# Optimization experiments

Hardware: AMD Instinct MI355X
Metric: run time of the kernel (lower is better)

## Reference

```python
import jax, jax.numpy as jnp
import numpy as np

F = 6      # num_factors (== nodes per sample)
H = 32     # hidden_dim
B = 65536  # batch of samples (vectorized version of the per-sample Python loop)


def setup_inputs() -> dict:
    key = jax.random.key(0)
    ks = jax.random.split(key, 20)
    p = lambda k, shape: (jax.random.normal(k, shape, dtype=jnp.float32) * 0.1)
    inp = {
        "factors": jax.random.normal(ks[0], (B, F, F), dtype=jnp.float32),
        # CausalStructureLearner.node_encoder: Linear(F, H)
        "Wn": p(ks[1], (F, H)), "bn": p(ks[2], (H,)),
        # edge_predictor: Linear(2H, H) -> ReLU -> Linear(H, 1) -> Sigmoid
        "We1": p(ks[3], (2 * H, H)), "be1": p(ks[4], (H,)),
        "We2": p(ks[5], (H, 1)), "be2": p(ks[6], (1,)),
        # DynamicsPredictor.dynamics_net: F->H->H->F
        "Wd1": p(ks[7], (F, H)), "bd1": p(ks[8], (H,)),
        "Wd2": p(ks[9], (H, H)), "bd2": p(ks[10], (H,)),
        "Wd3": p(ks[11], (H, F)), "bd3": p(ks[12], (F,)),
        # AnomalyScorer.score_net: 3F->32->16->1 -> Sigmoid
        "Ws1": p(ks[13], (3 * F, 32)), "bs1": p(ks[14], (32,)),
        "Ws2": p(ks[15], (32, 16)), "bs2": p(ks[16], (16,)),
        "Ws3": p(ks[17], (16, 1)), "bs3": p(ks[18], (1,)),
    }
    return inp


def reference(factors, Wn, bn, We1, be1, We2, be2,
              Wd1, bd1, Wd2, bd2, Wd3, bd3,
              Ws1, bs1, Ws2, bs2, Ws3, bs3):
    # --- CausalStructureLearner (vectorized pairwise edge scoring) ---
    nf = factors @ Wn + bn                                  # [B, F, H]
    src = jnp.broadcast_to(nf[:, :, None, :], (B, F, F, H))  # node i
    dst = jnp.broadcast_to(nf[:, None, :, :], (B, F, F, H))  # node j
    pair = jnp.concatenate([src, dst], axis=-1)             # [B, F, F, 2H]
    eh = jax.nn.relu(pair @ We1 + be1)                       # [B, F, F, H]
    adj = jax.nn.sigmoid((eh @ We2 + be2)[..., 0])           # [B, F, F]
    adj = adj * (1.0 - jnp.eye(F, dtype=adj.dtype))          # zero diagonal

    # --- DynamicsPredictor: (adj @ factors.T).T == factors @ adj^T ---
    structured = jnp.einsum('bij,bnj->bni', adj, factors)    # [B, F(nodes), F]
    h = jax.nn.relu(structured @ Wd1 + bd1)
    h = jax.nn.relu(h @ Wd2 + bd2)
    pred = h @ Wd3 + bd3                                     # [B, F, F]

    # --- AnomalyScorer ---
    diff = jnp.abs(factors - pred)
    si = jnp.concatenate([factors, pred, diff], axis=-1)     # [B, F, 3F]
    s = jax.nn.relu(si @ Ws1 + bs1)
    s = jax.nn.relu(s @ Ws2 + bs2)
    s = jax.nn.sigmoid(s @ Ws3 + bs3)                        # [B, F, 1]
    scores = jnp.mean(s, axis=(1, 2))                        # [B]

    return adj, pred, scores
```

## Files before the change

### kernel.cpp

```cpp
#include <hip/hip_runtime.h>
#include <math.h>

#define NT  256
#define SPB 84

#define O_REC  0
#define O_WD1  512
#define O_BD1  704
#define O_WD2  736
#define O_BD2  1760
#define O_WD3T 1792
#define O_BD3  1984
#define O_WS1  1992
#define O_BS1  2568
#define O_WS2  2600
#define O_BS2  3112
#define O_WS3  3128
#define O_MISC 3144
#define W_TOT  3148

#define ADJ_STRIDE 52

__device__ __forceinline__ float sigmoidf_(float x) {
    return 1.0f / (1.0f + __expf(-x));
}

__global__ __launch_bounds__(NT, 1) void fused3_kernel(
        const float* __restrict__ factors,
        const float* __restrict__ Wn,  const float* __restrict__ bn,
        const float* __restrict__ We1, const float* __restrict__ be1,
        const float* __restrict__ We2, const float* __restrict__ be2,
        const float* __restrict__ Wd1, const float* __restrict__ bd1,
        const float* __restrict__ Wd2, const float* __restrict__ bd2,
        const float* __restrict__ Wd3, const float* __restrict__ bd3,
        const float* __restrict__ Ws1, const float* __restrict__ bs1,
        const float* __restrict__ Ws2, const float* __restrict__ bs2,
        const float* __restrict__ Ws3, const float* __restrict__ bs3,
        float* __restrict__ adj_out, float* __restrict__ pred_out,
        float* __restrict__ scores, int B) {
    __shared__ float Wsh[W_TOT];
    __shared__ float adj_s[SPB * ADJ_STRIDE];
    __shared__ float sc_s[SPB * 6];

    const int t = threadIdx.x;
    const int s = t / 3;
    const int n = t - s * 3;
    const int b = blockIdx.x * SPB + s;
    const bool act = (t < SPB * 3);
    const int sl_ = (s < SPB) ? s : (SPB - 1);
    const bool bv = act && (b < B);

    float fall[36], fi0[6], fi1[6];
    #pragma unroll
    for (int q = 0; q < 36; ++q) fall[q] = 0.f;
    #pragma unroll
    for (int m = 0; m < 6; ++m) { fi0[m] = 0.f; fi1[m] = 0.f; }
    if (bv) {
        const float* f = factors + (size_t)b * 36;
        #pragma unroll
        for (int q = 0; q < 9; ++q) {
            float4 v = reinterpret_cast<const float4*>(f)[q];
            fall[q*4+0] = v.x; fall[q*4+1] = v.y; fall[q*4+2] = v.z; fall[q*4+3] = v.w;
        }
        const float* fr0 = f + n * 6;
        const float* fr1 = fr0 + 18;
        #pragma unroll
        for (int q = 0; q < 3; ++q) {
            float2 v0 = reinterpret_cast<const float2*>(fr0)[q];
            float2 v1 = reinterpret_cast<const float2*>(fr1)[q];
            fi0[q*2+0] = v0.x; fi0[q*2+1] = v0.y;
            fi1[q*2+0] = v1.x; fi1[q*2+1] = v1.y;
        }
    }

    #pragma unroll
    for (int e0 = 0; e0 < 512; e0 += NT) {
        int e = e0 + t;
        int h = e >> 4, sl = e & 15;
        float val = 0.0f;
        if (sl < 6) {
            #pragma unroll
            for (int k = 0; k < 32; ++k) val = fmaf(Wn[sl*32+k], We1[k*32+h], val);
        } else if (sl < 12) {
            int m = sl - 6;
            #pragma unroll
            for (int k = 0; k < 32; ++k) val = fmaf(Wn[m*32+k], We1[(32+k)*32+h], val);
        } else if (sl == 12) {
            #pragma unroll
            for (int k = 0; k < 32; ++k) val = fmaf(bn[k], We1[k*32+h] + We1[(32+k)*32+h], val);
            val += be1[h];
        } else if (sl == 13) {
            val = We2[h];
        }
        Wsh[O_REC + e] = val;
    }
    for (int i = t; i < 192;  i += NT) Wsh[O_WD1 + i] = Wd1[i];
    for (int i = t; i < 1024; i += NT) Wsh[O_WD2 + i] = Wd2[i];
    for (int i = t; i < 192;  i += NT) { int j = i >> 5, k = i & 31; Wsh[O_WD3T + i] = Wd3[k*6 + j]; }
    for (int i = t; i < 576;  i += NT) Wsh[O_WS1 + i] = Ws1[i];
    for (int i = t; i < 512;  i += NT) Wsh[O_WS2 + i] = Ws2[i];
    if (t < 32) Wsh[O_BD1 + t] = bd1[t];
    if (t < 32) Wsh[O_BD2 + t] = bd2[t];
    if (t < 6)  Wsh[O_BD3 + t] = bd3[t];
    if (t < 32) Wsh[O_BS1 + t] = bs1[t];
    if (t < 16) Wsh[O_BS2 + t] = bs2[t];
    if (t < 16) Wsh[O_WS3 + t] = Ws3[t];
    if (t == 0) { Wsh[O_MISC] = bs3[0]; Wsh[O_MISC + 1] = be2[0]; }
    __syncthreads();

    float av0[6], av1[6];
    {
        float acc0[6] = {0.f,0.f,0.f,0.f,0.f,0.f};
        float acc1[6] = {0.f,0.f,0.f,0.f,0.f,0.f};
        #pragma unroll 2
        for (int h = 0; h < 32; ++h) {
            const float* r = &Wsh[O_REC + (h << 4)];
            const float4 r0 = *reinterpret_cast<const float4*>(&r[0]);
            const float4 r1 = *reinterpret_cast<const float4*>(&r[4]);
            const float4 r2 = *reinterpret_cast<const float4*>(&r[8]);
            const float4 r3 = *reinterpret_cast<const float4*>(&r[12]);
            float uh0 = r3.x, uh1 = r3.x;
            uh0 = fmaf(fi0[0], r0.x, uh0); uh1 = fmaf(fi1[0], r0.x, uh1);
            uh0 = fmaf(fi0[1], r0.y, uh0); uh1 = fmaf(fi1[1], r0.y, uh1);
            uh0 = fmaf(fi0[2], r0.z, uh0); uh1 = fmaf(fi1[2], r0.z, uh1);
            uh0 = fmaf(fi0[3], r0.w, uh0); uh1 = fmaf(fi1[3], r0.w, uh1);
            uh0 = fmaf(fi0[4], r1.x, uh0); uh1 = fmaf(fi1[4], r1.x, uh1);
            uh0 = fmaf(fi0[5], r1.y, uh0); uh1 = fmaf(fi1[5], r1.y, uh1);
            const float w2 = r3.y;
            #pragma unroll
            for (int j = 0; j < 6; ++j) {
                float vj =      fall[j*6+0] * r1.z;
                vj = fmaf(fall[j*6+1], r1.w, vj);
                vj = fmaf(fall[j*6+2], r2.x, vj);
                vj = fmaf(fall[j*6+3], r2.y, vj);
                vj = fmaf(fall[j*6+4], r2.z, vj);
                vj = fmaf(fall[j*6+5], r2.w, vj);
                acc0[j] = fmaf(fmaxf(uh0 + vj, 0.f), w2, acc0[j]);
                acc1[j] = fmaf(fmaxf(uh1 + vj, 0.f), w2, acc1[j]);
            }
        }
        const float b2 = Wsh[O_MISC + 1];
        #pragma unroll
        for (int j = 0; j < 6; ++j) {
            av0[j] = (j == n)     ? 0.f : sigmoidf_(acc0[j] + b2);
            av1[j] = (j == n + 3) ? 0.f : sigmoidf_(acc1[j] + b2);
        }
    }
    if (act) {
        float* as = &adj_s[sl_ * ADJ_STRIDE];
        *reinterpret_cast<float4*>(&as[n*8])       = make_float4(av0[0], av0[1], av0[2], av0[3]);
        *reinterpret_cast<float2*>(&as[n*8+4])     = make_float2(av0[4], av0[5]);
        *reinterpret_cast<float4*>(&as[(n+3)*8])   = make_float4(av1[0], av1[1], av1[2], av1[3]);
        *reinterpret_cast<float2*>(&as[(n+3)*8+4]) = make_float2(av1[4], av1[5]);
    }
    if (bv) {
        float* ao = adj_out + (size_t)b * 36 + n * 6;
        *reinterpret_cast<float2*>(&ao[0])  = make_float2(av0[0], av0[1]);
        *reinterpret_cast<float2*>(&ao[2])  = make_float2(av0[2], av0[3]);
        *reinterpret_cast<float2*>(&ao[4])  = make_float2(av0[4], av0[5]);
        *reinterpret_cast<float2*>(&ao[18]) = make_float2(av1[0], av1[1]);
        *reinterpret_cast<float2*>(&ao[20]) = make_float2(av1[2], av1[3]);
        *reinterpret_cast<float2*>(&ao[22]) = make_float2(av1[4], av1[5]);
    }
    __syncthreads();

    float pra[6], prb[6];
    float h2a[32], h2b[32];
    {
        float st0[6], st1[6];
        {
            const float* as = &adj_s[sl_ * ADJ_STRIDE];
            #pragma unroll
            for (int i = 0; i < 6; ++i) {
                const float4 qa = *reinterpret_cast<const float4*>(&as[i*8]);
                const float2 qb = *reinterpret_cast<const float2*>(&as[i*8+4]);
                float v = fi0[0] * qa.x;
                v = fmaf(fi0[1], qa.y, v); v = fmaf(fi0[2], qa.z, v);
                v = fmaf(fi0[3], qa.w, v); v = fmaf(fi0[4], qb.x, v);
                v = fmaf(fi0[5], qb.y, v);
                st0[i] = v;
                float w = fi1[0] * qa.x;
                w = fmaf(fi1[1], qa.y, w); w = fmaf(fi1[2], qa.z, w);
                w = fmaf(fi1[3], qa.w, w); w = fmaf(fi1[4], qb.x, w);
                w = fmaf(fi1[5], qb.y, w);
                st1[i] = w;
            }
        }

        float h1a[32], h1b[32];
        #pragma unroll
        for (int o4 = 0; o4 < 8; ++o4) {
            const float4 v = *reinterpret_cast<const float4*>(&Wsh[O_BD1 + o4*4]);
            h1a[o4*4+0] = v.x; h1a[o4*4+1] = v.y; h1a[o4*4+2] = v.z; h1a[o4*4+3] = v.w;
            h1b[o4*4+0] = v.x; h1b[o4*4+1] = v.y; h1b[o4*4+2] = v.z; h1b[o4*4+3] = v.w;
        }
        #pragma unroll
        for (int m = 0; m < 6; ++m) {
            const float sa = st0[m], sb = st1[m];
            #pragma unroll
            for (int o4 = 0; o4 < 8; ++o4) {
                const float4 w = *reinterpret_cast<const float4*>(&Wsh[O_WD1 + m*32 + o4*4]);
                h1a[o4*4+0] = fmaf(sa, w.x, h1a[o4*4+0]); h1b[o4*4+0] = fmaf(sb, w.x, h1b[o4*4+0]);
                h1a[o4*4+1] = fmaf(sa, w.y, h1a[o4*4+1]); h1b[o4*4+1] = fmaf(sb, w.y, h1b[o4*4+1]);
                h1a[o4*4+2] = fmaf(sa, w.z, h1a[o4*4+2]); h1b[o4*4+2] = fmaf(sb, w.z, h1b[o4*4+2]);
                h1a[o4*4+3] = fmaf(sa, w.w, h1a[o4*4+3]); h1b[o4*4+3] = fmaf(sb, w.w, h1b[o4*4+3]);
            }
        }
        #pragma unroll
        for (int o = 0; o < 32; ++o) { h1a[o] = fmaxf(h1a[o], 0.f); h1b[o] = fmaxf(h1b[o], 0.f); }

        #pragma unroll
        for (int o4 = 0; o4 < 8; ++o4) {
            const float4 v = *reinterpret_cast<const float4*>(&Wsh[O_BD2 + o4*4]);
            h2a[o4*4+0] = v.x; h2a[o4*4+1] = v.y; h2a[o4*4+2] = v.z; h2a[o4*4+3] = v.w;
            h2b[o4*4+0] = v.x; h2b[o4*4+1] = v.y; h2b[o4*4+2] = v.z; h2b[o4*4+3] = v.w;
        }
        #pragma unroll
        for (int k = 0; k < 32; ++k) {
            const float xa = h1a[k], xb = h1b[k];
            #pragma unroll
            for (int o4 = 0; o4 < 8; ++o4) {
                const float4 w = *reinterpret_cast<const float4*>(&Wsh[O_WD2 + k*32 + o4*4]);
                h2a[o4*4+0] = fmaf(xa, w.x, h2a[o4*4+0]); h2b[o4*4+0] = fmaf(xb, w.x, h2b[o4*4+0]);
                h2a[o4*4+1] = fmaf(xa, w.y, h2a[o4*4+1]); h2b[o4*4+1] = fmaf(xb, w.y, h2b[o4*4+1]);
                h2a[o4*4+2] = fmaf(xa, w.z, h2a[o4*4+2]); h2b[o4*4+2] = fmaf(xb, w.z, h2b[o4*4+2]);
                h2a[o4*4+3] = fmaf(xa, w.w, h2a[o4*4+3]); h2b[o4*4+3] = fmaf(xb, w.w, h2b[o4*4+3]);
            }
        }
        #pragma unroll
        for (int o = 0; o < 32; ++o) { h2a[o] = fmaxf(h2a[o], 0.f); h2b[o] = fmaxf(h2b[o], 0.f); }
    }

    #pragma unroll
    for (int j = 0; j < 6; ++j) {
        float va = Wsh[O_BD3 + j], vb = va;
        #pragma unroll
        for (int k4 = 0; k4 < 8; ++k4) {
            const float4 w = *reinterpret_cast<const float4*>(&Wsh[O_WD3T + j*32 + k4*4]);
            va = fmaf(h2a[k4*4+0], w.x, va); vb = fmaf(h2b[k4*4+0], w.x, vb);
            va = fmaf(h2a[k4*4+1], w.y, va); vb = fmaf(h2b[k4*4+1], w.y, vb);
            va = fmaf(h2a[k4*4+2], w.z, va); vb = fmaf(h2b[k4*4+2], w.z, vb);
            va = fmaf(h2a[k4*4+3], w.w, va); vb = fmaf(h2b[k4*4+3], w.w, vb);
        }
        pra[j] = va; prb[j] = vb;
    }
    if (bv) {
        float* po = pred_out + (size_t)b * 36 + n * 6;
        *reinterpret_cast<float2*>(&po[0])  = make_float2(pra[0], pra[1]);
        *reinterpret_cast<float2*>(&po[2])  = make_float2(pra[2], pra[3]);
        *reinterpret_cast<float2*>(&po[4])  = make_float2(pra[4], pra[5]);
        *reinterpret_cast<float2*>(&po[18]) = make_float2(prb[0], prb[1]);
        *reinterpret_cast<float2*>(&po[20]) = make_float2(prb[2], prb[3]);
        *reinterpret_cast<float2*>(&po[22]) = make_float2(prb[4], prb[5]);
    }

    {
        float dfa[6], dfb[6];
        #pragma unroll
        for (int j = 0; j < 6; ++j) { dfa[j] = fabsf(fi0[j] - pra[j]); dfb[j] = fabsf(fi1[j] - prb[j]); }

        float s1a[32], s1b[32];
        #pragma unroll
        for (int o4 = 0; o4 < 8; ++o4) {
            const float4 v = *reinterpret_cast<const float4*>(&Wsh[O_BS1 + o4*4]);
            s1a[o4*4+0] = v.x; s1a[o4*4+1] = v.y; s1a[o4*4+2] = v.z; s1a[o4*4+3] = v.w;
            s1b[o4*4+0] = v.x; s1b[o4*4+1] = v.y; s1b[o4*4+2] = v.z; s1b[o4*4+3] = v.w;
        }
        #pragma unroll
        for (int m = 0; m < 6; ++m) {
            const float aa = fi0[m], pa = pra[m], da = dfa[m];
            const float ab = fi1[m], pb = prb[m], db = dfb[m];
            #pragma unroll
            for (int o4 = 0; o4 < 8; ++o4) {
                const float4 wa = *reinterpret_cast<const float4*>(&Wsh[O_WS1 + m*32 + o4*4]);
                const float4 wp = *reinterpret_cast<const float4*>(&Wsh[O_WS1 + (6+m)*32 + o4*4]);
                const float4 wd = *reinterpret_cast<const float4*>(&Wsh[O_WS1 + (12+m)*32 + o4*4]);
                s1a[o4*4+0] = fmaf(aa, wa.x, fmaf(pa, wp.x, fmaf(da, wd.x, s1a[o4*4+0])));
                s1b[o4*4+0] = fmaf(ab, wa.x, fmaf(pb, wp.x, fmaf(db, wd.x, s1b[o4*4+0])));
                s1a[o4*4+1] = fmaf(aa, wa.y, fmaf(pa, wp.y, fmaf(da, wd.y, s1a[o4*4+1])));
                s1b[o4*4+1] = fmaf(ab, wa.y, fmaf(pb, wp.y, fmaf(db, wd.y, s1b[o4*4+1])));
                s1a[o4*4+2] = fmaf(aa, wa.z, fmaf(pa, wp.z, fmaf(da, wd.z, s1a[o4*4+2])));
                s1b[o4*4+2] = fmaf(ab, wa.z, fmaf(pb, wp.z, fmaf(db, wd.z, s1b[o4*4+2])));
                s1a[o4*4+3] = fmaf(aa, wa.w, fmaf(pa, wp.w, fmaf(da, wd.w, s1a[o4*4+3])));
                s1b[o4*4+3] = fmaf(ab, wa.w, fmaf(pb, wp.w, fmaf(db, wd.w, s1b[o4*4+3])));
            }
        }
        #pragma unroll
        for (int o = 0; o < 32; ++o) { s1a[o] = fmaxf(s1a[o], 0.f); s1b[o] = fmaxf(s1b[o], 0.f); }

        float s2a[16], s2b[16];
        #pragma unroll
        for (int o4 = 0; o4 < 4; ++o4) {
            const float4 v = *reinterpret_cast<const float4*>(&Wsh[O_BS2 + o4*4]);
            s2a[o4*4+0] = v.x; s2a[o4*4+1] = v.y; s2a[o4*4+2] = v.z; s2a[o4*4+3] = v.w;
            s2b[o4*4+0] = v.x; s2b[o4*4+1] = v.y; s2b[o4*4+2] = v.z; s2b[o4*4+3] = v.w;
        }
        #pragma unroll
        for (int k = 0; k < 32; ++k) {
            const float xa = s1a[k], xb = s1b[k];
            #pragma unroll
            for (int o4 = 0; o4 < 4; ++o4) {
                const float4 w = *reinterpret_cast<const float4*>(&Wsh[O_WS2 + k*16 + o4*4]);
                s2a[o4*4+0] = fmaf(xa, w.x, s2a[o4*4+0]); s2b[o4*4+0] = fmaf(xb, w.x, s2b[o4*4+0]);
                s2a[o4*4+1] = fmaf(xa, w.y, s2a[o4*4+1]); s2b[o4*4+1] = fmaf(xb, w.y, s2b[o4*4+1]);
                s2a[o4*4+2] = fmaf(xa, w.z, s2a[o4*4+2]); s2b[o4*4+2] = fmaf(xb, w.z, s2b[o4*4+2]);
                s2a[o4*4+3] = fmaf(xa, w.w, s2a[o4*4+3]); s2b[o4*4+3] = fmaf(xb, w.w, s2b[o4*4+3]);
            }
        }
        #pragma unroll
        for (int o = 0; o < 16; ++o) { s2a[o] = fmaxf(s2a[o], 0.f); s2b[o] = fmaxf(s2b[o], 0.f); }

        float s3a = Wsh[O_MISC], s3b = s3a;
        #pragma unroll
        for (int k4 = 0; k4 < 4; ++k4) {
            const float4 w = *reinterpret_cast<const float4*>(&Wsh[O_WS3 + k4*4]);
            s3a = fmaf(s2a[k4*4+0], w.x, s3a); s3b = fmaf(s2b[k4*4+0], w.x, s3b);
            s3a = fmaf(s2a[k4*4+1], w.y, s3a); s3b = fmaf(s2b[k4*4+1], w.y, s3b);
            s3a = fmaf(s2a[k4*4+2], w.z, s3a); s3b = fmaf(s2b[k4*4+2], w.z, s3b);
            s3a = fmaf(s2a[k4*4+3], w.w, s3a); s3b = fmaf(s2b[k4*4+3], w.w, s3b);
        }
        if (act) {
            sc_s[sl_*6 + n]     = sigmoidf_(s3a);
            sc_s[sl_*6 + n + 3] = sigmoidf_(s3b);
        }
    }
    __syncthreads();

    if (bv && n == 0) {
        float sum = sc_s[sl_*6+0] + sc_s[sl_*6+1] + sc_s[sl_*6+2]
                  + sc_s[sl_*6+3] + sc_s[sl_*6+4] + sc_s[sl_*6+5];
        scores[b] = sum * (1.0f / 6.0f);
    }
}

extern "C" void kernel_launch(void* const* d_in, const int* in_sizes, int n_in,
                              void* d_out, int out_size, void* d_ws, size_t ws_size,
                              hipStream_t stream) {
    const float* factors = (const float*)d_in[0];
    const float* Wn  = (const float*)d_in[1];
    const float* bn  = (const float*)d_in[2];
    const float* We1 = (const float*)d_in[3];
    const float* be1 = (const float*)d_in[4];
    const float* We2 = (const float*)d_in[5];
    const float* be2 = (const float*)d_in[6];
    const float* Wd1 = (const float*)d_in[7];
    const float* bd1 = (const float*)d_in[8];
    const float* Wd2 = (const float*)d_in[9];
    const float* bd2 = (const float*)d_in[10];
    const float* Wd3 = (const float*)d_in[11];
    const float* bd3 = (const float*)d_in[12];
    const float* Ws1 = (const float*)d_in[13];
    const float* bs1 = (const float*)d_in[14];
    const float* Ws2 = (const float*)d_in[15];
    const float* bs2 = (const float*)d_in[16];
    const float* Ws3 = (const float*)d_in[17];
    const float* bs3 = (const float*)d_in[18];

    int B = in_sizes[0] / 36;

    float* adj_out  = (float*)d_out;
    float* pred_out = (float*)d_out + (size_t)B * 36;
    float* scores   = (float*)d_out + (size_t)B * 72;

    int nblocks = (B + SPB - 1) / SPB;
    hipLaunchKernelGGL(fused3_kernel, dim3(nblocks), dim3(NT), 0, stream,
                       factors, Wn, bn, We1, be1, We2, be2,
                       Wd1, bd1, Wd2, bd2, Wd3, bd3,
                       Ws1, bs1, Ws2, bs2, Ws3, bs3,
                       adj_out, pred_out, scores, B);
}
```

Baseline: 179.7 us.

## Precompute folded weights once in a prologue kernel and store them as fp16

A single-block prologue kernel now folds the node encoder into the edge MLP and packs every weight matrix as fp16 (biases stay fp32) into a workspace buffer. The main kernel loads that buffer with float4 copies instead of having each of ~780 blocks redo the 32-term weight folding and the scattered weight loads. Shared-memory weight reads shrink to half8 vectors that are converted to fp32 for the FMAs. This removes redundant per-block setup and halves LDS traffic for weights, in exchange for an extra kernel launch, conversion instructions in the inner loops and fp16 rounding of the weights.

```diff
diff --git a/kernel.cpp b/kernel.cpp
--- a/kernel.cpp
+++ b/kernel.cpp
@@ -1,23 +1,25 @@
 #include <hip/hip_runtime.h>
 #include <math.h>
 
+typedef _Float16 half8 __attribute__((ext_vector_type(8)));
+
 #define NT  256
 #define SPB 84
 
-#define O_REC  0
-#define O_WD1  512
-#define O_BD1  704
-#define O_WD2  736
-#define O_BD2  1760
-#define O_WD3T 1792
-#define O_BD3  1984
-#define O_WS1  1992
-#define O_BS1  2568
-#define O_WS2  2600
-#define O_BS2  3112
-#define O_WS3  3128
-#define O_MISC 3144
-#define W_TOT  3148
+#define FH_REC   0
+#define FH_WD1   256
+#define FH_WD2   352
+#define FH_WD3T  864
+#define FH_WS1   960
+#define FH_WS2   1248
+#define FH_WS3   1504
+#define FF_BD1   1512
+#define FF_BD2   1544
+#define FF_BD3   1576
+#define FF_BS1   1584
+#define FF_BS2   1616
+#define FF_MISC  1632
+#define W_TOTF   1640
 
 #define ADJ_STRIDE 52
 
@@ -25,8 +27,7 @@
     return 1.0f / (1.0f + __expf(-x));
 }
 
-__global__ __launch_bounds__(NT, 1) void fused3_kernel(
-        const float* __restrict__ factors,
+__global__ __launch_bounds__(512) void fold_kernel(
         const float* __restrict__ Wn,  const float* __restrict__ bn,
         const float* __restrict__ We1, const float* __restrict__ be1,
         const float* __restrict__ We2, const float* __restrict__ be2,
@@ -36,13 +37,69 @@
         const float* __restrict__ Ws1, const float* __restrict__ bs1,
         const float* __restrict__ Ws2, const float* __restrict__ bs2,
         const float* __restrict__ Ws3, const float* __restrict__ bs3,
+        float* __restrict__ cat) {
+    _Float16* cath = (_Float16*)cat;
+    const int t = threadIdx.x;
+    {
+        const int h = t >> 4, sl = t & 15;
+        float val = 0.0f;
+        if (sl < 6) {
+            #pragma unroll
+            for (int k = 0; k < 32; ++k) val = fmaf(Wn[sl*32+k], We1[k*32+h], val);
+        } else if (sl < 12) {
+            const int m = sl - 6;
+            #pragma unroll
+            for (int k = 0; k < 32; ++k) val = fmaf(Wn[m*32+k], We1[(32+k)*32+h], val);
+        } else if (sl == 12) {
+            #pragma unroll
+            for (int k = 0; k < 32; ++k) val = fmaf(bn[k], We1[k*32+h] + We1[(32+k)*32+h], val);
+            val += be1[h];
+        } else if (sl == 13) {
+            val = We2[h];
+        }
+        cath[h*16 + sl] = (_Float16)val;
+    }
+    for (int i = 512 + t; i < 3024; i += 512) {
+        float v = 0.0f;
+        if      (i < 704)  v = Wd1[i - 512];
+        else if (i < 1728) v = Wd2[i - 704];
+        else if (i < 1920) { const int q = i - 1728; v = Wd3[(q & 31)*6 + (q >> 5)]; }
+        else if (i < 2496) v = Ws1[i - 1920];
+        else if (i < 3008) v = Ws2[i - 2496];
+        else               v = Ws3[i - 3008];
+        cath[i] = (_Float16)v;
+    }
+    if (t < 128) {
+        const int q = t;
+        float v = 0.0f;
+        if      (q < 32)  v = bd1[q];
+        else if (q < 64)  v = bd2[q-32];
+        else if (q < 70)  v = bd3[q-64];
+        else if (q < 72)  v = 0.0f;
+        else if (q < 104) v = bs1[q-72];
+        else if (q < 120) v = bs2[q-104];
+        else if (q == 120) v = bs3[0];
+        else if (q == 121) v = be2[0];
+        cat[1512 + q] = v;
+    }
+}
+
+__global__ __launch_bounds__(NT, 1) void fused5_kernel(
+        const float* __restrict__ factors, const float* __restrict__ cat,
         float* __restrict__ adj_out, float* __restrict__ pred_out,
         float* __restrict__ scores, int B) {
-    __shared__ float Wsh[W_TOT];
-    __shared__ float adj_s[SPB * ADJ_STRIDE];
+    __shared__ __align__(16) float Wsh[W_TOTF];
+    __shared__ __align__(16) float adj_s[SPB * ADJ_STRIDE];
     __shared__ float sc_s[SPB * 6];
 
     const int t = threadIdx.x;
+    #pragma unroll
+    for (int i0 = 0; i0 < 2048; i0 += NT * 4) {
+        const int i = i0 + t * 4;
+        if (i < W_TOTF)
+            *reinterpret_cast<float4*>(&Wsh[i]) = *reinterpret_cast<const float4*>(&cat[i]);
+    }
+
     const int s = t / 3;
     const int n = t - s * 3;
     const int b = blockIdx.x * SPB + s;
@@ -52,98 +109,58 @@
 
     float fall[36], fi0[6], fi1[6];
     #pragma unroll
-    for (int q = 0; q < 36; ++q) fall[q] = 0.f;
-    #pragma unroll
-    for (int m = 0; m < 6; ++m) { fi0[m] = 0.f; fi1[m] = 0.f; }
+    for (int q = 0; q < 36; ++q) fall[q] = 0.0f;
+    #pragma unroll
+    for (int m = 0; m < 6; ++m) { fi0[m] = 0.0f; fi1[m] = 0.0f; }
     if (bv) {
         const float* f = factors + (size_t)b * 36;
         #pragma unroll
         for (int q = 0; q < 9; ++q) {
-            float4 v = reinterpret_cast<const float4*>(f)[q];
+            const float4 v = reinterpret_cast<const float4*>(f)[q];
             fall[q*4+0] = v.x; fall[q*4+1] = v.y; fall[q*4+2] = v.z; fall[q*4+3] = v.w;
         }
-        const float* fr0 = f + n * 6;
-        const float* fr1 = fr0 + 18;
-        #pragma unroll
-        for (int q = 0; q < 3; ++q) {
-            float2 v0 = reinterpret_cast<const float2*>(fr0)[q];
-            float2 v1 = reinterpret_cast<const float2*>(fr1)[q];
-            fi0[q*2+0] = v0.x; fi0[q*2+1] = v0.y;
-            fi1[q*2+0] = v1.x; fi1[q*2+1] = v1.y;
-        }
-    }
-
-    #pragma unroll
-    for (int e0 = 0; e0 < 512; e0 += NT) {
-        int e = e0 + t;
-        int h = e >> 4, sl = e & 15;
-        float val = 0.0f;
-        if (sl < 6) {
-            #pragma unroll
-            for (int k = 0; k < 32; ++k) val = fmaf(Wn[sl*32+k], We1[k*32+h], val);
-        } else if (sl < 12) {
-            int m = sl - 6;
-            #pragma unroll
-            for (int k = 0; k < 32; ++k) val = fmaf(Wn[m*32+k], We1[(32+k)*32+h], val);
-        } else if (sl == 12) {
-            #pragma unroll
-            for (int k = 0; k < 32; ++k) val = fmaf(bn[k], We1[k*32+h] + We1[(32+k)*32+h], val);
-            val += be1[h];
-        } else if (sl == 13) {
-            val = We2[h];
-        }
-        Wsh[O_REC + e] = val;
-    }
-    for (int i = t; i < 192;  i += NT) Wsh[O_WD1 + i] = Wd1[i];
-    for (int i = t; i < 1024; i += NT) Wsh[O_WD2 + i] = Wd2[i];
-    for (int i = t; i < 192;  i += NT) { int j = i >> 5, k = i & 31; Wsh[O_WD3T + i] = Wd3[k*6 + j]; }
-    for (int i = t; i < 576;  i += NT) Wsh[O_WS1 + i] = Ws1[i];
-    for (int i = t; i < 512;  i += NT) Wsh[O_WS2 + i] = Ws2[i];
-    if (t < 32) Wsh[O_BD1 + t] = bd1[t];
-    if (t < 32) Wsh[O_BD2 + t] = bd2[t];
-    if (t < 6)  Wsh[O_BD3 + t] = bd3[t];
-    if (t < 32) Wsh[O_BS1 + t] = bs1[t];
-    if (t < 16) Wsh[O_BS2 + t] = bs2[t];
-    if (t < 16) Wsh[O_WS3 + t] = Ws3[t];
-    if (t == 0) { Wsh[O_MISC] = bs3[0]; Wsh[O_MISC + 1] = be2[0]; }
+        #pragma unroll
+        for (int m = 0; m < 6; ++m) { fi0[m] = fall[n*6 + m]; fi1[m] = fall[(n+3)*6 + m]; }
+    }
     __syncthreads();
 
     float av0[6], av1[6];
     {
         float acc0[6] = {0.f,0.f,0.f,0.f,0.f,0.f};
         float acc1[6] = {0.f,0.f,0.f,0.f,0.f,0.f};
-        #pragma unroll 2
+        #pragma unroll 4
         for (int h = 0; h < 32; ++h) {
-            const float* r = &Wsh[O_REC + (h << 4)];
-            const float4 r0 = *reinterpret_cast<const float4*>(&r[0]);
-            const float4 r1 = *reinterpret_cast<const float4*>(&r[4]);
-            const float4 r2 = *reinterpret_cast<const float4*>(&r[8]);
-            const float4 r3 = *reinterpret_cast<const float4*>(&r[12]);
-            float uh0 = r3.x, uh1 = r3.x;
-            uh0 = fmaf(fi0[0], r0.x, uh0); uh1 = fmaf(fi1[0], r0.x, uh1);
-            uh0 = fmaf(fi0[1], r0.y, uh0); uh1 = fmaf(fi1[1], r0.y, uh1);
-            uh0 = fmaf(fi0[2], r0.z, uh0); uh1 = fmaf(fi1[2], r0.z, uh1);
-            uh0 = fmaf(fi0[3], r0.w, uh0); uh1 = fmaf(fi1[3], r0.w, uh1);
-            uh0 = fmaf(fi0[4], r1.x, uh0); uh1 = fmaf(fi1[4], r1.x, uh1);
-            uh0 = fmaf(fi0[5], r1.y, uh0); uh1 = fmaf(fi1[5], r1.y, uh1);
-            const float w2 = r3.y;
+            const half8 ha = *reinterpret_cast<const half8*>(&Wsh[FH_REC + h*8]);
+            const half8 hb = *reinterpret_cast<const half8*>(&Wsh[FH_REC + h*8 + 4]);
+            const float A0=(float)ha[0], A1=(float)ha[1], A2=(float)ha[2];
+            const float A3=(float)ha[3], A4=(float)ha[4], A5=(float)ha[5];
+            const float B0=(float)ha[6], B1=(float)ha[7], B2=(float)hb[0];
+            const float B3=(float)hb[1], B4=(float)hb[2], B5=(float)hb[3];
+            const float c0=(float)hb[4], w2=(float)hb[5];
+            float uh0 = c0, uh1 = c0;
+            uh0 = fmaf(fi0[0], A0, uh0); uh1 = fmaf(fi1[0], A0, uh1);
+            uh0 = fmaf(fi0[1], A1, uh0); uh1 = fmaf(fi1[1], A1, uh1);
+            uh0 = fmaf(fi0[2], A2, uh0); uh1 = fmaf(fi1[2], A2, uh1);
+            uh0 = fmaf(fi0[3], A3, uh0); uh1 = fmaf(fi1[3], A3, uh1);
+            uh0 = fmaf(fi0[4], A4, uh0); uh1 = fmaf(fi1[4], A4, uh1);
+            uh0 = fmaf(fi0[5], A5, uh0); uh1 = fmaf(fi1[5], A5, uh1);
             #pragma unroll
             for (int j = 0; j < 6; ++j) {
-                float vj =      fall[j*6+0] * r1.z;
-                vj = fmaf(fall[j*6+1], r1.w, vj);
-                vj = fmaf(fall[j*6+2], r2.x, vj);
-                vj = fmaf(fall[j*6+3], r2.y, vj);
-                vj = fmaf(fall[j*6+4], r2.z, vj);
-                vj = fmaf(fall[j*6+5], r2.w, vj);
-                acc0[j] = fmaf(fmaxf(uh0 + vj, 0.f), w2, acc0[j]);
-                acc1[j] = fmaf(fmaxf(uh1 + vj, 0.f), w2, acc1[j]);
-            }
-        }
-        const float b2 = Wsh[O_MISC + 1];
+                float vj = fall[j*6+0] * B0;
+                vj = fmaf(fall[j*6+1], B1, vj);
+                vj = fmaf(fall[j*6+2], B2, vj);
+                vj = fmaf(fall[j*6+3], B3, vj);
+                vj = fmaf(fall[j*6+4], B4, vj);
+                vj = fmaf(fall[j*6+5], B5, vj);
+                acc0[j] = fmaf(fmaxf(uh0 + vj, 0.0f), w2, acc0[j]);
+                acc1[j] = fmaf(fmaxf(uh1 + vj, 0.0f), w2, acc1[j]);
+            }
+        }
+        const float b2 = Wsh[FF_MISC + 1];
         #pragma unroll
         for (int j = 0; j < 6; ++j) {
-            av0[j] = (j == n)     ? 0.f : sigmoidf_(acc0[j] + b2);
-            av1[j] = (j == n + 3) ? 0.f : sigmoidf_(acc1[j] + b2);
+            av0[j] = (j == n)     ? 0.0f : sigmoidf_(acc0[j] + b2);
+            av1[j] = (j == n + 3) ? 0.0f : sigmoidf_(acc1[j] + b2);
         }
     }
     if (act) {
@@ -164,83 +181,90 @@
     }
     __syncthreads();
 
+    float st0[6], st1[6];
+    {
+        const float* as = &adj_s[sl_ * ADJ_STRIDE];
+        #pragma unroll
+        for (int i = 0; i < 6; ++i) {
+            const float4 qa = *reinterpret_cast<const float4*>(&as[i*8]);
+            const float2 qb = *reinterpret_cast<const float2*>(&as[i*8+4]);
+            float v = fi0[0] * qa.x;
+            v = fmaf(fi0[1], qa.y, v); v = fmaf(fi0[2], qa.z, v);
+            v = fmaf(fi0[3], qa.w, v); v = fmaf(fi0[4], qb.x, v);
+            v = fmaf(fi0[5], qb.y, v);
+            st0[i] = v;
+            float w = fi1[0] * qa.x;
+            w = fmaf(fi1[1], qa.y, w); w = fmaf(fi1[2], qa.z, w);
+            w = fmaf(fi1[3], qa.w, w); w = fmaf(fi1[4], qb.x, w);
+            w = fmaf(fi1[5], qb.y, w);
+            st1[i] = w;
+        }
+    }
+
+    float h1a[32], h1b[32];
+    #pragma unroll
+    for (int o4 = 0; o4 < 8; ++o4) {
+        const float4 v = *reinterpret_cast<const float4*>(&Wsh[FF_BD1 + o4*4]);
+        h1a[o4*4+0] = v.x; h1a[o4*4+1] = v.y; h1a[o4*4+2] = v.z; h1a[o4*4+3] = v.w;
+        h1b[o4*4+0] = v.x; h1b[o4*4+1] = v.y; h1b[o4*4+2] = v.z; h1b[o4*4+3] = v.w;
+    }
+    #pragma unroll
+    for (int m = 0; m < 6; ++m) {
+        const float xa = st0[m], xb = st1[m];
+        #pragma unroll
+        for (int q = 0; q < 4; ++q) {
+            const half8 w = *reinterpret_cast<const half8*>(&Wsh[FH_WD1 + m*16 + q*4]);
+            #pragma unroll
+            for (int e = 0; e < 8; ++e) {
+                const float wf = (float)w[e];
+                h1a[q*8+e] = fmaf(xa, wf, h1a[q*8+e]);
+                h1b[q*8+e] = fmaf(xb, wf, h1b[q*8+e]);
+            }
+        }
+    }
+    #pragma unroll
+    for (int o = 0; o < 32; ++o) { h1a[o] = fmaxf(h1a[o], 0.0f); h1b[o] = fmaxf(h1b[o], 0.0f); }
+
+    float h2a[32], h2b[32];
+    #pragma unroll
+    for (int o4 = 0; o4 < 8; ++o4) {
+        const float4 v = *reinterpret_cast<const float4*>(&Wsh[FF_BD2 + o4*4]);
+        h2a[o4*4+0] = v.x; h2a[o4*4+1] = v.y; h2a[o4*4+2] = v.z; h2a[o4*4+3] = v.w;
+        h2b[o4*4+0] = v.x; h2b[o4*4+1] = v.y; h2b[o4*4+2] = v.z; h2b[o4*4+3] = v.w;
+    }
+    #pragma unroll
+    for (int p = 0; p < 2; ++p) {
+        #pragma unroll
+        for (int k = 0; k < 32; ++k) {
+            const half8 w0 = *reinterpret_cast<const half8*>(&Wsh[FH_WD2 + k*16 + p*8]);
+            const half8 w1 = *reinterpret_cast<const half8*>(&Wsh[FH_WD2 + k*16 + p*8 + 4]);
+            const float xa = h1a[k], xb = h1b[k];
+            #pragma unroll
+            for (int e = 0; e < 8; ++e) {
+                const float we0 = (float)w0[e], we1 = (float)w1[e];
+                h2a[p*16+e]   = fmaf(xa, we0, h2a[p*16+e]);
+                h2b[p*16+e]   = fmaf(xb, we0, h2b[p*16+e]);
+                h2a[p*16+8+e] = fmaf(xa, we1, h2a[p*16+8+e]);
+                h2b[p*16+8+e] = fmaf(xb, we1, h2b[p*16+8+e]);
+            }
+        }
+    }
+    #pragma unroll
+    for (int o = 0; o < 32; ++o) { h2a[o] = fmaxf(h2a[o], 0.0f); h2b[o] = fmaxf(h2b[o], 0.0f); }
+
     float pra[6], prb[6];
-    float h2a[32], h2b[32];
-    {
-        float st0[6], st1[6];
-        {
-            const float* as = &adj_s[sl_ * ADJ_STRIDE];
-            #pragma unroll
-            for (int i = 0; i < 6; ++i) {
-                const float4 qa = *reinterpret_cast<const float4*>(&as[i*8]);
-                const float2 qb = *reinterpret_cast<const float2*>(&as[i*8+4]);
-                float v = fi0[0] * qa.x;
-                v = fmaf(fi0[1], qa.y, v); v = fmaf(fi0[2], qa.z, v);
-                v = fmaf(fi0[3], qa.w, v); v = fmaf(fi0[4], qb.x, v);
-                v = fmaf(fi0[5], qb.y, v);
-                st0[i] = v;
-                float w = fi1[0] * qa.x;
-                w = fmaf(fi1[1], qa.y, w); w = fmaf(fi1[2], qa.z, w);
-                w = fmaf(fi1[3], qa.w, w); w = fmaf(fi1[4], qb.x, w);
-                w = fmaf(fi1[5], qb.y, w);
-                st1[i] = w;
-            }
-        }
-
-        float h1a[32], h1b[32];
-        #pragma unroll
-        for (int o4 = 0; o4 < 8; ++o4) {
-            const float4 v = *reinterpret_cast<const float4*>(&Wsh[O_BD1 + o4*4]);
-            h1a[o4*4+0] = v.x; h1a[o4*4+1] = v.y; h1a[o4*4+2] = v.z; h1a[o4*4+3] = v.w;
-            h1b[o4*4+0] = v.x; h1b[o4*4+1] = v.y; h1b[o4*4+2] = v.z; h1b[o4*4+3] = v.w;
-        }
-        #pragma unroll
-        for (int m = 0; m < 6; ++m) {
-            const float sa = st0[m], sb = st1[m];
-            #pragma unroll
-            for (int o4 = 0; o4 < 8; ++o4) {
-                const float4 w = *reinterpret_cast<const float4*>(&Wsh[O_WD1 + m*32 + o4*4]);
-                h1a[o4*4+0] = fmaf(sa, w.x, h1a[o4*4+0]); h1b[o4*4+0] = fmaf(sb, w.x, h1b[o4*4+0]);
-                h1a[o4*4+1] = fmaf(sa, w.y, h1a[o4*4+1]); h1b[o4*4+1] = fmaf(sb, w.y, h1b[o4*4+1]);
-                h1a[o4*4+2] = fmaf(sa, w.z, h1a[o4*4+2]); h1b[o4*4+2] = fmaf(sb, w.z, h1b[o4*4+2]);
-                h1a[o4*4+3] = fmaf(sa, w.w, h1a[o4*4+3]); h1b[o4*4+3] = fmaf(sb, w.w, h1b[o4*4+3]);
-            }
-        }
-        #pragma unroll
-        for (int o = 0; o < 32; ++o) { h1a[o] = fmaxf(h1a[o], 0.f); h1b[o] = fmaxf(h1b[o], 0.f); }
-
-        #pragma unroll
-        for (int o4 = 0; o4 < 8; ++o4) {
-            const float4 v = *reinterpret_cast<const float4*>(&Wsh[O_BD2 + o4*4]);
-            h2a[o4*4+0] = v.x; h2a[o4*4+1] = v.y; h2a[o4*4+2] = v.z; h2a[o4*4+3] = v.w;
-            h2b[o4*4+0] = v.x; h2b[o4*4+1] = v.y; h2b[o4*4+2] = v.z; h2b[o4*4+3] = v.w;
-        }
-        #pragma unroll
-        for (int k = 0; k < 32; ++k) {
-            const float xa = h1a[k], xb = h1b[k];
-            #pragma unroll
-            for (int o4 = 0; o4 < 8; ++o4) {
-                const float4 w = *reinterpret_cast<const float4*>(&Wsh[O_WD2 + k*32 + o4*4]);
-                h2a[o4*4+0] = fmaf(xa, w.x, h2a[o4*4+0]); h2b[o4*4+0] = fmaf(xb, w.x, h2b[o4*4+0]);
-                h2a[o4*4+1] = fmaf(xa, w.y, h2a[o4*4+1]); h2b[o4*4+1] = fmaf(xb, w.y, h2b[o4*4+1]);
-                h2a[o4*4+2] = fmaf(xa, w.z, h2a[o4*4+2]); h2b[o4*4+2] = fmaf(xb, w.z, h2b[o4*4+2]);
-                h2a[o4*4+3] = fmaf(xa, w.w, h2a[o4*4+3]); h2b[o4*4+3] = fmaf(xb, w.w, h2b[o4*4+3]);
-            }
-        }
-        #pragma unroll
-        for (int o = 0; o < 32; ++o) { h2a[o] = fmaxf(h2a[o], 0.f); h2b[o] = fmaxf(h2b[o], 0.f); }
-    }
-
     #pragma unroll
     for (int j = 0; j < 6; ++j) {
-        float va = Wsh[O_BD3 + j], vb = va;
-        #pragma unroll
-        for (int k4 = 0; k4 < 8; ++k4) {
-            const float4 w = *reinterpret_cast<const float4*>(&Wsh[O_WD3T + j*32 + k4*4]);
-            va = fmaf(h2a[k4*4+0], w.x, va); vb = fmaf(h2b[k4*4+0], w.x, vb);
-            va = fmaf(h2a[k4*4+1], w.y, va); vb = fmaf(h2b[k4*4+1], w.y, vb);
-            va = fmaf(h2a[k4*4+2], w.z, va); vb = fmaf(h2b[k4*4+2], w.z, vb);
-            va = fmaf(h2a[k4*4+3], w.w, va); vb = fmaf(h2b[k4*4+3], w.w, vb);
+        float va = Wsh[FF_BD3 + j], vb = va;
+        #pragma unroll
+        for (int q = 0; q < 4; ++q) {
+            const half8 w = *reinterpret_cast<const half8*>(&Wsh[FH_WD3T + j*16 + q*4]);
+            #pragma unroll
+            for (int e = 0; e < 8; ++e) {
+                const float wf = (float)w[e];
+                va = fmaf(h2a[q*8+e], wf, va);
+                vb = fmaf(h2b[q*8+e], wf, vb);
+            }
         }
         pra[j] = va; prb[j] = vb;
     }
@@ -254,70 +278,71 @@
         *reinterpret_cast<float2*>(&po[22]) = make_float2(prb[4], prb[5]);
     }
 
+    float dfa[6], dfb[6];
+    #pragma unroll
+    for (int j = 0; j < 6; ++j) { dfa[j] = fabsf(fi0[j] - pra[j]); dfb[j] = fabsf(fi1[j] - prb[j]); }
+
+    float s1a[32], s1b[32];
+    #pragma unroll
+    for (int o4 = 0; o4 < 8; ++o4) {
+        const float4 v = *reinterpret_cast<const float4*>(&Wsh[FF_BS1 + o4*4]);
+        s1a[o4*4+0] = v.x; s1a[o4*4+1] = v.y; s1a[o4*4+2] = v.z; s1a[o4*4+3] = v.w;
+        s1b[o4*4+0] = v.x; s1b[o4*4+1] = v.y; s1b[o4*4+2] = v.z; s1b[o4*4+3] = v.w;
+    }
+    #pragma unroll
+    for (int m = 0; m < 6; ++m) {
+        const float aa = fi0[m], pa = pra[m], da = dfa[m];
+        const float ab = fi1[m], pb = prb[m], db = dfb[m];
+        #pragma unroll
+        for (int q = 0; q < 4; ++q) {
+            const half8 wa = *reinterpret_cast<const half8*>(&Wsh[FH_WS1 + m*16 + q*4]);
+            const half8 wp = *reinterpret_cast<const half8*>(&Wsh[FH_WS1 + (6+m)*16 + q*4]);
+            const half8 wd = *reinterpret_cast<const half8*>(&Wsh[FH_WS1 + (12+m)*16 + q*4]);
+            #pragma unroll
+            for (int e = 0; e < 8; ++e) {
+                const int o = q*8 + e;
+                const float x1 = (float)wa[e], x2 = (float)wp[e], x3 = (float)wd[e];
+                s1a[o] = fmaf(aa, x1, fmaf(pa, x2, fmaf(da, x3, s1a[o])));
+                s1b[o] = fmaf(ab, x1, fmaf(pb, x2, fmaf(db, x3, s1b[o])));
+            }
+        }
+    }
+    #pragma unroll
+    for (int o = 0; o < 32; ++o) { s1a[o] = fmaxf(s1a[o], 0.0f); s1b[o] = fmaxf(s1b[o], 0.0f); }
+
+    float s2a[16], s2b[16];
+    #pragma unroll
+    for (int o4 = 0; o4 < 4; ++o4) {
+        const float4 v = *reinterpret_cast<const float4*>(&Wsh[FF_BS2 + o4*4]);
+        s2a[o4*4+0] = v.x; s2a[o4*4+1] = v.y; s2a[o4*4+2] = v.z; s2a[o4*4+3] = v.w;
+        s2b[o4*4+0] = v.x; s2b[o4*4+1] = v.y; s2b[o4*4+2] = v.z; s2b[o4*4+3] = v.w;
+    }
+    #pragma unroll
+    for (int k = 0; k < 32; ++k) {
+        const half8 w0 = *reinterpret_cast<const half8*>(&Wsh[FH_WS2 + k*8]);
+        const half8 w1 = *reinterpret_cast<const half8*>(&Wsh[FH_WS2 + k*8 + 4]);
+        const float xa = s1a[k], xb = s1b[k];
+        #pragma unroll
+        for (int e = 0; e < 8; ++e) {
+            const float we0 = (float)w0[e], we1 = (float)w1[e];
+            s2a[e]   = fmaf(xa, we0, s2a[e]);
+            s2b[e]   = fmaf(xb, we0, s2b[e]);
+            s2a[8+e] = fmaf(xa, we1, s2a[8+e]);
+            s2b[8+e] = fmaf(xb, we1, s2b[8+e]);
+        }
+    }
+    #pragma unroll
+    for (int o = 0; o < 16; ++o) { s2a[o] = fmaxf(s2a[o], 0.0f); s2b[o] = fmaxf(s2b[o], 0.0f); }
+
     {
-        float dfa[6], dfb[6];
-        #pragma unroll
-        for (int j = 0; j < 6; ++j) { dfa[j] = fabsf(fi0[j] - pra[j]); dfb[j] = fabsf(fi1[j] - prb[j]); }
-
-        float s1a[32], s1b[32];
-        #pragma unroll
-        for (int o4 = 0; o4 < 8; ++o4) {
-            const float4 v = *reinterpret_cast<const float4*>(&Wsh[O_BS1 + o4*4]);
-            s1a[o4*4+0] = v.x; s1a[o4*4+1] = v.y; s1a[o4*4+2] = v.z; s1a[o4*4+3] = v.w;
-            s1b[o4*4+0] = v.x; s1b[o4*4+1] = v.y; s1b[o4*4+2] = v.z; s1b[o4*4+3] = v.w;
-        }
-        #pragma unroll
-        for (int m = 0; m < 6; ++m) {
-            const float aa = fi0[m], pa = pra[m], da = dfa[m];
-            const float ab = fi1[m], pb = prb[m], db = dfb[m];
-            #pragma unroll
-            for (int o4 = 0; o4 < 8; ++o4) {
-                const float4 wa = *reinterpret_cast<const float4*>(&Wsh[O_WS1 + m*32 + o4*4]);
-                const float4 wp = *reinterpret_cast<const float4*>(&Wsh[O_WS1 + (6+m)*32 + o4*4]);
-                const float4 wd = *reinterpret_cast<const float4*>(&Wsh[O_WS1 + (12+m)*32 + o4*4]);
-                s1a[o4*4+0] = fmaf(aa, wa.x, fmaf(pa, wp.x, fmaf(da, wd.x, s1a[o4*4+0])));
-                s1b[o4*4+0] = fmaf(ab, wa.x, fmaf(pb, wp.x, fmaf(db, wd.x, s1b[o4*4+0])));
-                s1a[o4*4+1] = fmaf(aa, wa.y, fmaf(pa, wp.y, fmaf(da, wd.y, s1a[o4*4+1])));
-                s1b[o4*4+1] = fmaf(ab, wa.y, fmaf(pb, wp.y, fmaf(db, wd.y, s1b[o4*4+1])));
-                s1a[o4*4+2] = fmaf(aa, wa.z, fmaf(pa, wp.z, fmaf(da, wd.z, s1a[o4*4+2])));
-                s1b[o4*4+2] = fmaf(ab, wa.z, fmaf(pb, wp.z, fmaf(db, wd.z, s1b[o4*4+2])));
-                s1a[o4*4+3] = fmaf(aa, wa.w, fmaf(pa, wp.w, fmaf(da, wd.w, s1a[o4*4+3])));
-                s1b[o4*4+3] = fmaf(ab, wa.w, fmaf(pb, wp.w, fmaf(db, wd.w, s1b[o4*4+3])));
-            }
-        }
-        #pragma unroll
-        for (int o = 0; o < 32; ++o) { s1a[o] = fmaxf(s1a[o], 0.f); s1b[o] = fmaxf(s1b[o], 0.f); }
-
-        float s2a[16], s2b[16];
-        #pragma unroll
-        for (int o4 = 0; o4 < 4; ++o4) {
-            const float4 v = *reinterpret_cast<const float4*>(&Wsh[O_BS2 + o4*4]);
-            s2a[o4*4+0] = v.x; s2a[o4*4+1] = v.y; s2a[o4*4+2] = v.z; s2a[o4*4+3] = v.w;
-            s2b[o4*4+0] = v.x; s2b[o4*4+1] = v.y; s2b[o4*4+2] = v.z; s2b[o4*4+3] = v.w;
-        }
-        #pragma unroll
-        for (int k = 0; k < 32; ++k) {
-            const float xa = s1a[k], xb = s1b[k];
-            #pragma unroll
-            for (int o4 = 0; o4 < 4; ++o4) {
-                const float4 w = *reinterpret_cast<const float4*>(&Wsh[O_WS2 + k*16 + o4*4]);
-                s2a[o4*4+0] = fmaf(xa, w.x, s2a[o4*4+0]); s2b[o4*4+0] = fmaf(xb, w.x, s2b[o4*4+0]);
-                s2a[o4*4+1] = fmaf(xa, w.y, s2a[o4*4+1]); s2b[o4*4+1] = fmaf(xb, w.y, s2b[o4*4+1]);
-                s2a[o4*4+2] = fmaf(xa, w.z, s2a[o4*4+2]); s2b[o4*4+2] = fmaf(xb, w.z, s2b[o4*4+2]);
-                s2a[o4*4+3] = fmaf(xa, w.w, s2a[o4*4+3]); s2b[o4*4+3] = fmaf(xb, w.w, s2b[o4*4+3]);
-            }
-        }
-        #pragma unroll
-        for (int o = 0; o < 16; ++o) { s2a[o] = fmaxf(s2a[o], 0.f); s2b[o] = fmaxf(s2b[o], 0.f); }
-
-        float s3a = Wsh[O_MISC], s3b = s3a;
-        #pragma unroll
-        for (int k4 = 0; k4 < 4; ++k4) {
-            const float4 w = *reinterpret_cast<const float4*>(&Wsh[O_WS3 + k4*4]);
-            s3a = fmaf(s2a[k4*4+0], w.x, s3a); s3b = fmaf(s2b[k4*4+0], w.x, s3b);
-            s3a = fmaf(s2a[k4*4+1], w.y, s3a); s3b = fmaf(s2b[k4*4+1], w.y, s3b);
-            s3a = fmaf(s2a[k4*4+2], w.z, s3a); s3b = fmaf(s2b[k4*4+2], w.z, s3b);
-            s3a = fmaf(s2a[k4*4+3], w.w, s3a); s3b = fmaf(s2b[k4*4+3], w.w, s3b);
+        const half8 w0 = *reinterpret_cast<const half8*>(&Wsh[FH_WS3]);
+        const half8 w1 = *reinterpret_cast<const half8*>(&Wsh[FH_WS3 + 4]);
+        float s3a = Wsh[FF_MISC], s3b = s3a;
+        #pragma unroll
+        for (int e = 0; e < 8; ++e) {
+            const float we0 = (float)w0[e], we1 = (float)w1[e];
+            s3a = fmaf(s2a[e], we0, s3a);   s3b = fmaf(s2b[e], we0, s3b);
+            s3a = fmaf(s2a[8+e], we1, s3a); s3b = fmaf(s2b[8+e], we1, s3b);
         }
         if (act) {
             sc_s[sl_*6 + n]     = sigmoidf_(s3a);
@@ -327,8 +352,8 @@
     __syncthreads();
 
     if (bv && n == 0) {
-        float sum = sc_s[sl_*6+0] + sc_s[sl_*6+1] + sc_s[sl_*6+2]
-                  + sc_s[sl_*6+3] + sc_s[sl_*6+4] + sc_s[sl_*6+5];
+        const float sum = sc_s[sl_*6+0] + sc_s[sl_*6+1] + sc_s[sl_*6+2]
+                        + sc_s[sl_*6+3] + sc_s[sl_*6+4] + sc_s[sl_*6+5];
         scores[b] = sum * (1.0f / 6.0f);
     }
 }
@@ -356,16 +381,19 @@
     const float* Ws3 = (const float*)d_in[17];
     const float* bs3 = (const float*)d_in[18];
 
-    int B = in_sizes[0] / 36;
+    const int B = in_sizes[0] / 36;
 
     float* adj_out  = (float*)d_out;
     float* pred_out = (float*)d_out + (size_t)B * 36;
     float* scores   = (float*)d_out + (size_t)B * 72;
-
-    int nblocks = (B + SPB - 1) / SPB;
-    hipLaunchKernelGGL(fused3_kernel, dim3(nblocks), dim3(NT), 0, stream,
-                       factors, Wn, bn, We1, be1, We2, be2,
+    float* cat      = (float*)d_ws;
+
+    hipLaunchKernelGGL(fold_kernel, dim3(1), dim3(512), 0, stream,
+                       Wn, bn, We1, be1, We2, be2,
                        Wd1, bd1, Wd2, bd2, Wd3, bd3,
-                       Ws1, bs1, Ws2, bs2, Ws3, bs3,
-                       adj_out, pred_out, scores, B);
+                       Ws1, bs1, Ws2, bs2, Ws3, bs3, cat);
+
+    const int nblocks = (B + SPB - 1) / SPB;
+    hipLaunchKernelGGL(fused5_kernel, dim3(nblocks), dim3(NT), 0, stream,
+                       factors, cat, adj_out, pred_out, scores, B);
 }
```

Result: faster. 174.2 us (-3.1%).
